# Performance work log

Measured on AMD Instinct MI355X. Metric: run time of the kernel, lower is better.

Reference implementation:

```python
import jax, jax.numpy as jnp
import numpy as np

B, L, S, E, D = 16, 2048, 2048, 64, 64

def setup_inputs() -> dict:
    key = jax.random.key(0)
    k1, k2, k3, k4 = jax.random.split(key, 4)
    queries = jax.random.normal(k1, (B, L, E), dtype=jnp.float32)
    keys = jax.random.normal(k2, (B, S, E), dtype=jnp.float32)
    values = jax.random.normal(k3, (B, S, D), dtype=jnp.float32)
    mlp = jax.random.normal(k4, (L, L), dtype=jnp.float32)  # learned seq-mix matrix
    return {"queries": queries, "keys": keys, "values": values, "mlp": mlp}

def reference(queries, keys, values, mlp):
    # scale = 1/sqrt(E) (self.scale is None)
    E_dim = queries.shape[-1]
    scale = 1.0 / jnp.sqrt(jnp.asarray(E_dim, dtype=queries.dtype))
    # scores: [B, L, S]
    scores = jnp.einsum('ble,bse->bls', queries, keys)
    # dropout omitted (eval mode / attention_dropout=0)
    A = jax.nn.softmax(scale * scores, axis=-1)
    # attention output: [B, L, D]
    V = jnp.einsum('bls,bsd->bld', A, values)
    # learned sequence-mixing: [B, L, D] -> [B, P, D] with P == L
    out = jnp.einsum('bld,pl->bpd', V, mlp)
    return out
```

## Files before the change

kernel.cpp:

```cpp
#include <hip/hip_runtime.h>

#define NB 16
#define NL 2048
#define NS 2048
#define NE 64
#define ND 64

typedef float floatx4 __attribute__((ext_vector_type(4)));
typedef _Float16 half8 __attribute__((ext_vector_type(8)));
typedef __fp16 half2v __attribute__((ext_vector_type(2)));

union H8 { half8 v; half2v h2[4]; };

__device__ __forceinline__ half8 cvt8(floatx4 a, floatx4 b) {
  H8 h;
  h.h2[0] = __builtin_amdgcn_cvt_pkrtz(a[0], a[1]);
  h.h2[1] = __builtin_amdgcn_cvt_pkrtz(a[2], a[3]);
  h.h2[2] = __builtin_amdgcn_cvt_pkrtz(b[0], b[1]);
  h.h2[3] = __builtin_amdgcn_cvt_pkrtz(b[2], b[3]);
  return h.v;
}

__device__ __forceinline__ void async16(void* l, const void* g) {
  __builtin_amdgcn_global_load_lds((__attribute__((address_space(1))) void*)g,
                                   (__attribute__((address_space(3))) void*)l, 16, 0, 0);
}

__device__ __forceinline__ int kinv(int y) {
  return (y & 0x23) | ((y & 8) << 1) | ((y & 4) << 1) | ((y & 16) >> 2);
}

__global__ __launch_bounds__(256) void prep_k(const float* __restrict__ V,
                                              const float* __restrict__ K,
                                              _Float16* __restrict__ Vt,
                                              _Float16* __restrict__ Kh,
                                              int do_k) {
  __shared__ __align__(16) _Float16 Vl[64][72];
  const int bid = blockIdx.x;
  const int t = threadIdx.x;

  if (bid < 512) {
    const int b = bid >> 5;
    const int s0 = (bid & 31) * 64;
    {
      int sl = t & 63;
      int dg = t >> 6;
      const float* src = V + ((size_t)(b * NS + s0 + sl)) * ND + dg * 16;
      int x = kinv(sl);
      #pragma unroll
      for (int c = 0; c < 4; ++c) {
        floatx4 v = *(const floatx4*)(src + c * 4);
        #pragma unroll
        for (int e = 0; e < 4; ++e) Vl[dg * 16 + c * 4 + e][x] = (_Float16)v[e];
      }
    }
    __syncthreads();
    {
      int d = t & 63;
      int xg = t >> 6;
      int dk = (d & 7) << 3;
      #pragma unroll
      for (int h = 0; h < 2; ++h) {
        int x = xg * 16 + h * 8;
        half8 v = *(const half8*)&Vl[d][x];
        *(half8*)(Vt + ((size_t)(b * ND + d)) * NS + s0 + (x ^ dk)) = v;
      }
    }
  } else {
    if (!do_k) return;
    int c = (bid - 512) * 256 + t;
    int j = c & 7;
    int s = (c >> 3) & (NS - 1);
    int b = c >> 14;
    const float* src = K + ((size_t)(b * NS + s)) * NE + j * 8;
    half8 h = cvt8(*(const floatx4*)src, *(const floatx4*)(src + 4));
    *(half8*)(Kh + ((size_t)(b * NS + s)) * NE + (j ^ (s & 7)) * 8) = h;
  }
}

template<bool KH16>
__global__ __launch_bounds__(512) void attn_k(const float* __restrict__ Q,
                                              const void* __restrict__ Ksrc,
                                              const _Float16* __restrict__ Vtp,
                                              _Float16* __restrict__ Vatt,
                                              const float* __restrict__ Mf,
                                              _Float16* __restrict__ Mh) {
  __shared__ __align__(16) char smem[98304];
  const int tid = threadIdx.x;
  const int wid = tid >> 6, lane = tid & 63;
  const int lr = lane & 15, lg = lane >> 4;
  const int g = wid & 1;
  const int qh = wid >> 1;
  const int L = blockIdx.y * 16 + blockIdx.x;
  const int b = (L & 7) * 2 + ((L >> 3) & 1);
  const int qx = L >> 4;
  const int qbase = qx * 128 + qh * 32;
  const _Float16* Kh = (const _Float16*)Ksrc;
  const float* Kf = (const float*)Ksrc;

  constexpr float SC = 0.18033688f;
  half8 qf[2][2];
  #pragma unroll
  for (int sub = 0; sub < 2; ++sub)
    #pragma unroll
    for (int kk = 0; kk < 2; ++kk) {
      const float* qp = Q + ((size_t)(b * NL + qbase + sub * 16 + lr)) * NE + kk * 32 + lg * 8;
      floatx4 a = *(const floatx4*)qp, c = *(const floatx4*)(qp + 4);
      qf[sub][kk] = cvt8(a * SC, c * SC);
    }

  half8 ones;
  #pragma unroll
  for (int i = 0; i < 8; ++i) ones[i] = (_Float16)1.0f;

  floatx4 oacc[2][4], lacc[2];
  #pragma unroll
  for (int s = 0; s < 2; ++s) {
    lacc[s] = (floatx4){0.f, 0.f, 0.f, 0.f};
    #pragma unroll
    for (int m = 0; m < 4; ++m) oacc[s][m] = (floatx4){0.f, 0.f, 0.f, 0.f};
  }

  int kOff[4][2], vOff[2][4];
  #pragma unroll
  for (int mt = 0; mt < 4; ++mt)
    #pragma unroll
    for (int kk = 0; kk < 2; ++kk) {
      int row = g * 64 + mt * 16 + lr, col = kk * 32 + lg * 8;
      kOff[mt][kk] = (row * 128 + col * 2) ^ ((row & 7) << 4);
    }
  #pragma unroll
  for (int kk = 0; kk < 2; ++kk)
    #pragma unroll
    for (int mt = 0; mt < 4; ++mt) {
      int row = mt * 16 + lr;
      vOff[kk][mt] = row * 256 + g * 128 + (((kk * 32 + lg * 8) * 2) ^ ((row & 7) << 4));
    }

  auto stageV = [&](int buf, int s0) {
    #pragma unroll
    for (int i = 0; i < 2; ++i) {
      int co = (wid * 2 + i) * 1024;
      int o = co + lane * 16;
      int row = o >> 8, c16 = (o >> 4) & 15;
      async16(smem + 49152 + buf * 16384 + co,
              Vtp + ((size_t)(b * ND + row)) * NS + s0 + c16 * 8);
    }
  };
  auto stageK = [&](int buf, int s0) {
    if constexpr (KH16) {
      #pragma unroll
      for (int i = 0; i < 2; ++i) {
        int co = (wid * 2 + i) * 1024;
        int o = co + lane * 16;
        int row = o >> 7, c8 = (o >> 4) & 7;
        async16(smem + buf * 16384 + co,
                Kh + ((size_t)(b * NS + s0 + row)) * NE + c8 * 8);
      }
    } else {
      int row = tid >> 2, cg = (tid & 3) * 16;
      const float* kp = Kf + ((size_t)(b * NS + s0 + row)) * NE + cg;
      #pragma unroll
      for (int c = 0; c < 2; ++c) {
        half8 h = cvt8(*(const floatx4*)(kp + c * 8), *(const floatx4*)(kp + c * 8 + 4));
        int col = cg + c * 8;
        *(half8*)(smem + buf * 16384 + ((row * 128 + col * 2) ^ ((row & 7) << 4))) = h;
      }
    }
  };

  stageK(0, 0); stageV(0, 0);

  int br = 0;
  for (int t = 0; t < NS / 128; ++t) {
    int bn = (br == 2) ? 0 : br + 1;
    if (t + 1 < NS / 128) {
      stageK(bn, (t + 1) * 128); stageV(bn, (t + 1) * 128);
      if constexpr (KH16) {
        asm volatile("s_waitcnt vmcnt(4)" ::: "memory");
        __builtin_amdgcn_s_barrier();
      } else __syncthreads();
    } else {
      if constexpr (KH16) {
        asm volatile("s_waitcnt vmcnt(0)" ::: "memory");
        __builtin_amdgcn_s_barrier();
      } else __syncthreads();
    }

    const char* kb = smem + br * 16384;
    const char* vb = smem + 49152 + br * 16384;

    half8 kf[4][2];
    #pragma unroll
    for (int mt = 0; mt < 4; ++mt)
      #pragma unroll
      for (int kk = 0; kk < 2; ++kk)
        kf[mt][kk] = *(const half8*)(kb + kOff[mt][kk]);

    H8 bf[2][2];
    #pragma unroll
    for (int sub = 0; sub < 2; ++sub) {
      floatx4 sacc[4];
      #pragma unroll
      for (int mt = 0; mt < 4; ++mt) sacc[mt] = (floatx4){0.f, 0.f, 0.f, 0.f};
      __builtin_amdgcn_s_setprio(1);
      #pragma unroll
      for (int kk = 0; kk < 2; ++kk)
        #pragma unroll
        for (int mt = 0; mt < 4; ++mt)
          sacc[mt] = __builtin_amdgcn_mfma_f32_16x16x32_f16(kf[mt][kk], qf[sub][kk], sacc[mt], 0, 0, 0);
      __builtin_amdgcn_s_setprio(0);

      #pragma unroll
      for (int mt = 0; mt < 4; ++mt) {
        float p0 = __builtin_amdgcn_exp2f(sacc[mt][0]);
        float p1 = __builtin_amdgcn_exp2f(sacc[mt][1]);
        float p2 = __builtin_amdgcn_exp2f(sacc[mt][2]);
        float p3 = __builtin_amdgcn_exp2f(sacc[mt][3]);
        bf[sub][mt >> 1].h2[(mt & 1) * 2]     = __builtin_amdgcn_cvt_pkrtz(p0, p1);
        bf[sub][mt >> 1].h2[(mt & 1) * 2 + 1] = __builtin_amdgcn_cvt_pkrtz(p2, p3);
      }
    }

    __builtin_amdgcn_s_setprio(1);
    #pragma unroll
    for (int kk = 0; kk < 2; ++kk) {
      #pragma unroll
      for (int mt = 0; mt < 4; ++mt) {
        half8 vt = *(const half8*)(vb + vOff[kk][mt]);
        oacc[0][mt] = __builtin_amdgcn_mfma_f32_16x16x32_f16(vt, bf[0][kk].v, oacc[0][mt], 0, 0, 0);
        oacc[1][mt] = __builtin_amdgcn_mfma_f32_16x16x32_f16(vt, bf[1][kk].v, oacc[1][mt], 0, 0, 0);
      }
      lacc[0] = __builtin_amdgcn_mfma_f32_16x16x32_f16(ones, bf[0][kk].v, lacc[0], 0, 0, 0);
      lacc[1] = __builtin_amdgcn_mfma_f32_16x16x32_f16(ones, bf[1][kk].v, lacc[1], 0, 0, 0);
    }
    __builtin_amdgcn_s_setprio(0);
    br = bn;
  }

  __syncthreads();

  {
    char* red = smem + qh * 12288;
    if (g == 1) {
      #pragma unroll
      for (int sub = 0; sub < 2; ++sub)
        #pragma unroll
        for (int mt = 0; mt < 4; ++mt)
          *(floatx4*)(red + lane * 144 + (sub * 4 + mt) * 16) = oacc[sub][mt];
      if (lg == 0) {
        *(float*)(red + 9216 + lr * 8) = lacc[0][0];
        *(float*)(red + 9216 + lr * 8 + 4) = lacc[1][0];
      }
    }
    __syncthreads();
    if (g == 0) {
      #pragma unroll
      for (int sub = 0; sub < 2; ++sub) {
        float lt = lacc[sub][0] + *(const float*)(red + 9216 + lr * 8 + sub * 4);
        float inv = __builtin_amdgcn_rcpf(lt);
        int l = qbase + sub * 16 + lr;
        #pragma unroll
        for (int mt = 0; mt < 4; ++mt) {
          floatx4 o = oacc[sub][mt] + *(const floatx4*)(red + lane * 144 + (sub * 4 + mt) * 16);
          #pragma unroll
          for (int r = 0; r < 4; ++r) {
            int d = mt * 16 + lg * 4 + r;
            int lsw = (l & ~63) | ((l & 63) ^ ((d & 7) << 3));
            Vatt[((size_t)(b * ND + d)) * NL + lsw] = (_Float16)(o[r] * inv);
          }
        }
      }
    }
  }

  if constexpr (KH16) {
    int mb = blockIdx.y * 16 + blockIdx.x;
    #pragma unroll
    for (int q = 0; q < 4; ++q) {
      int c = mb * 2048 + q * 512 + tid;
      int j = c & 255, p = c >> 8;
      const float* src = Mf + (size_t)p * NL + j * 8;
      half8 h = cvt8(*(const floatx4*)src, *(const floatx4*)(src + 4));
      int jo = (j & ~7) | ((j & 7) ^ (p & 7));
      *(half8*)(Mh + (size_t)p * NL + jo * 8) = h;
    }
  }
}

template<bool A16>
__global__ __launch_bounds__(256) void mix_k(const void* __restrict__ Asrc,
                                             const _Float16* __restrict__ Bsrc,
                                             float* __restrict__ out) {
  __shared__ __align__(16) char smem[65536];
  const int tid = threadIdx.x;
  const int wid = tid >> 6, lane = tid & 63;
  const int lr = lane & 15, lg = lane >> 4;
  const int kh = wid & 1;
  const int mw = wid >> 1;
  const int L = blockIdx.y * 32 + blockIdx.x;
  const int i = L >> 3;
  const int p0 = ((L & 7) * 4 + (i & 3)) * 64;
  const int b = i >> 2;
  const _Float16* Ah = (const _Float16*)Asrc;
  const float* Af = (const float*)Asrc;

  floatx4 acc[2][4];
  #pragma unroll
  for (int mt = 0; mt < 2; ++mt)
    #pragma unroll
    for (int nt = 0; nt < 4; ++nt) acc[mt][nt] = (floatx4){0.f, 0.f, 0.f, 0.f};

  auto stage = [&](int buf, int t) {
    int k0 = kh * (NL / 2) + t * 64;
    if constexpr (A16) {
      #pragma unroll
      for (int i2 = 0; i2 < 4; ++i2) {
        int co = (mw * 4 + i2) * 1024;
        int o = co + lane * 16;
        int row = o >> 7, c8 = (o >> 4) & 7;
        async16(smem + kh * 16384 + buf * 8192 + co,
                Ah + ((size_t)(p0 + row)) * NL + k0 + c8 * 8);
      }
    } else {
      int row = (lane & 31) + mw * 32, cg = (lane >> 5) * 32;
      const float* ap = Af + ((size_t)(p0 + row)) * NL + k0 + cg;
      #pragma unroll
      for (int c = 0; c < 4; ++c) {
        half8 h = cvt8(*(const floatx4*)(ap + c * 8), *(const floatx4*)(ap + c * 8 + 4));
        int col = cg + c * 8;
        *(half8*)(smem + kh * 16384 + buf * 8192 +
                  ((row * 128 + col * 2) ^ ((row & 7) << 4))) = h;
      }
    }
    #pragma unroll
    for (int i2 = 0; i2 < 4; ++i2) {
      int co = (mw * 4 + i2) * 1024;
      int o = co + lane * 16;
      int row = o >> 7, c8 = (o >> 4) & 7;
      async16(smem + 32768 + kh * 16384 + buf * 8192 + co,
              Bsrc + ((size_t)(b * ND + row)) * NL + k0 + c8 * 8);
    }
  };

  stage(0, 0);
  if constexpr (!A16) __syncthreads();

  for (int t = 0; t < 16; ++t) {
    int buf = t & 1;
    if constexpr (A16) {
      asm volatile("s_waitcnt vmcnt(0)" ::: "memory");
      __builtin_amdgcn_s_barrier();
      if (t + 1 < 16) stage(buf ^ 1, t + 1);
    } else {
      if (t + 1 < 16) { stage(buf ^ 1, t + 1); __syncthreads(); }
    }
    const char* ab = smem + kh * 16384 + buf * 8192;
    const char* bb = smem + 32768 + kh * 16384 + buf * 8192;
    #pragma unroll
    for (int kk = 0; kk < 2; ++kk) {
      int col = kk * 32 + lg * 8;
      half8 af[2];
      #pragma unroll
      for (int mt = 0; mt < 2; ++mt) {
        int row = mw * 32 + mt * 16 + lr;
        af[mt] = *(const half8*)(ab + ((row * 128 + col * 2) ^ ((row & 7) << 4)));
      }
      __builtin_amdgcn_s_setprio(1);
      #pragma unroll
      for (int nt = 0; nt < 4; ++nt) {
        int row = nt * 16 + lr;
        half8 bfr = *(const half8*)(bb + ((row * 128 + col * 2) ^ ((row & 7) << 4)));
        #pragma unroll
        for (int mt = 0; mt < 2; ++mt)
          acc[mt][nt] = __builtin_amdgcn_mfma_f32_16x16x32_f16(af[mt], bfr, acc[mt][nt], 0, 0, 0);
      }
      __builtin_amdgcn_s_setprio(0);
    }
    if constexpr (!A16) __syncthreads();
  }

  __syncthreads();

  if (kh == 1) {
    #pragma unroll
    for (int mt = 0; mt < 2; ++mt)
      #pragma unroll
      for (int nt = 0; nt < 4; ++nt) {
        int idx = mt * 4 + nt;
        *(floatx4*)(smem + mw * 8192 + lane * 128 + ((idx ^ (lane & 7)) * 16)) = acc[mt][nt];
      }
  }
  __syncthreads();
  if (kh == 0) {
    #pragma unroll
    for (int mt = 0; mt < 2; ++mt)
      #pragma unroll
      for (int nt = 0; nt < 4; ++nt) {
        int idx = mt * 4 + nt;
        acc[mt][nt] += *(const floatx4*)(smem + mw * 8192 + lane * 128 + ((idx ^ (lane & 7)) * 16));
        #pragma unroll
        for (int r = 0; r < 4; ++r) {
          int p = p0 + mw * 32 + mt * 16 + lg * 4 + r;
          int d = nt * 16 + lr;
          out[((size_t)(b * NL + p)) * ND + d] = acc[mt][nt][r];
        }
      }
  }
}

extern "C" void kernel_launch(void* const* d_in, const int* in_sizes, int n_in,
                              void* d_out, int out_size, void* d_ws, size_t ws_size,
                              hipStream_t stream) {
  (void)in_sizes; (void)n_in; (void)out_size;
  const float* Q = (const float*)d_in[0];
  const float* K = (const float*)d_in[1];
  const float* V = (const float*)d_in[2];
  const float* M = (const float*)d_in[3];
  float* out = (float*)d_out;

  char* ws = (char*)d_ws;
  _Float16* Vtp  = (_Float16*)ws;
  _Float16* Vatt = (_Float16*)(ws + (4u << 20));
  _Float16* Kh   = (_Float16*)(ws + (8u << 20));
  _Float16* Mh   = (_Float16*)(ws + (12u << 20));
  bool big = ws_size >= (size_t)(20u << 20);

  if (big) {
    prep_k<<<1536, 256, 0, stream>>>(V, K, Vtp, Kh, 1);
    attn_k<true><<<dim3(16, 16), 512, 0, stream>>>(Q, Kh, Vtp, Vatt, M, Mh);
    mix_k<true><<<dim3(32, 16), 256, 0, stream>>>(Mh, Vatt, out);
  } else {
    prep_k<<<512, 256, 0, stream>>>(V, K, Vtp, Kh, 0);
    attn_k<false><<<dim3(16, 16), 512, 0, stream>>>(Q, K, Vtp, Vatt, nullptr, nullptr);
    mix_k<false><<<dim3(32, 16), 256, 0, stream>>>(M, Vatt, out);
  }
}
```

Baseline: 51.83 us.

## Convert K to fp16 inside attention with register-prefetched loads, drop K prep pass

```diff
diff --git a/kernel.cpp b/kernel.cpp
--- a/kernel.cpp
+++ b/kernel.cpp
@@ -31,56 +31,41 @@
 }
 
 __global__ __launch_bounds__(256) void prep_k(const float* __restrict__ V,
-                                              const float* __restrict__ K,
-                                              _Float16* __restrict__ Vt,
-                                              _Float16* __restrict__ Kh,
-                                              int do_k) {
+                                              _Float16* __restrict__ Vt) {
   __shared__ __align__(16) _Float16 Vl[64][72];
   const int bid = blockIdx.x;
   const int t = threadIdx.x;
-
-  if (bid < 512) {
-    const int b = bid >> 5;
-    const int s0 = (bid & 31) * 64;
-    {
-      int sl = t & 63;
-      int dg = t >> 6;
-      const float* src = V + ((size_t)(b * NS + s0 + sl)) * ND + dg * 16;
-      int x = kinv(sl);
-      #pragma unroll
-      for (int c = 0; c < 4; ++c) {
-        floatx4 v = *(const floatx4*)(src + c * 4);
-        #pragma unroll
-        for (int e = 0; e < 4; ++e) Vl[dg * 16 + c * 4 + e][x] = (_Float16)v[e];
-      }
-    }
-    __syncthreads();
-    {
-      int d = t & 63;
-      int xg = t >> 6;
-      int dk = (d & 7) << 3;
-      #pragma unroll
-      for (int h = 0; h < 2; ++h) {
-        int x = xg * 16 + h * 8;
-        half8 v = *(const half8*)&Vl[d][x];
-        *(half8*)(Vt + ((size_t)(b * ND + d)) * NS + s0 + (x ^ dk)) = v;
-      }
-    }
-  } else {
-    if (!do_k) return;
-    int c = (bid - 512) * 256 + t;
-    int j = c & 7;
-    int s = (c >> 3) & (NS - 1);
-    int b = c >> 14;
-    const float* src = K + ((size_t)(b * NS + s)) * NE + j * 8;
-    half8 h = cvt8(*(const floatx4*)src, *(const floatx4*)(src + 4));
-    *(half8*)(Kh + ((size_t)(b * NS + s)) * NE + (j ^ (s & 7)) * 8) = h;
-  }
-}
-
-template<bool KH16>
+  const int b = bid >> 5;
+  const int s0 = (bid & 31) * 64;
+  {
+    int sl = t & 63;
+    int dg = t >> 6;
+    const float* src = V + ((size_t)(b * NS + s0 + sl)) * ND + dg * 16;
+    int x = kinv(sl);
+    #pragma unroll
+    for (int c = 0; c < 4; ++c) {
+      floatx4 v = *(const floatx4*)(src + c * 4);
+      #pragma unroll
+      for (int e = 0; e < 4; ++e) Vl[dg * 16 + c * 4 + e][x] = (_Float16)v[e];
+    }
+  }
+  __syncthreads();
+  {
+    int d = t & 63;
+    int xg = t >> 6;
+    int dk = (d & 7) << 3;
+    #pragma unroll
+    for (int h = 0; h < 2; ++h) {
+      int x = xg * 16 + h * 8;
+      half8 v = *(const half8*)&Vl[d][x];
+      *(half8*)(Vt + ((size_t)(b * ND + d)) * NS + s0 + (x ^ dk)) = v;
+    }
+  }
+}
+
+template<bool DOM>
 __global__ __launch_bounds__(512) void attn_k(const float* __restrict__ Q,
-                                              const void* __restrict__ Ksrc,
+                                              const float* __restrict__ Kf,
                                               const _Float16* __restrict__ Vtp,
                                               _Float16* __restrict__ Vatt,
                                               const float* __restrict__ Mf,
@@ -95,8 +80,6 @@
   const int b = (L & 7) * 2 + ((L >> 3) & 1);
   const int qx = L >> 4;
   const int qbase = qx * 128 + qh * 32;
-  const _Float16* Kh = (const _Float16*)Ksrc;
-  const float* Kf = (const float*)Ksrc;
 
   constexpr float SC = 0.18033688f;
   half8 qf[2][2];
@@ -136,6 +119,11 @@
       int row = mt * 16 + lr;
       vOff[kk][mt] = row * 256 + g * 128 + (((kk * 32 + lg * 8) * 2) ^ ((row & 7) << 4));
     }
+
+  const int krow = tid >> 2;
+  const int kcg = (tid & 3) * 16;
+  const int kw0 = (krow * 128 + kcg * 2) ^ ((krow & 7) << 4);
+  const int kw1 = (krow * 128 + (kcg + 8) * 2) ^ ((krow & 7) << 4);
 
   auto stageV = [&](int buf, int s0) {
     #pragma unroll
@@ -147,44 +135,31 @@
               Vtp + ((size_t)(b * ND + row)) * NS + s0 + c16 * 8);
     }
   };
-  auto stageK = [&](int buf, int s0) {
-    if constexpr (KH16) {
-      #pragma unroll
-      for (int i = 0; i < 2; ++i) {
-        int co = (wid * 2 + i) * 1024;
-        int o = co + lane * 16;
-        int row = o >> 7, c8 = (o >> 4) & 7;
-        async16(smem + buf * 16384 + co,
-                Kh + ((size_t)(b * NS + s0 + row)) * NE + c8 * 8);
-      }
-    } else {
-      int row = tid >> 2, cg = (tid & 3) * 16;
-      const float* kp = Kf + ((size_t)(b * NS + s0 + row)) * NE + cg;
-      #pragma unroll
-      for (int c = 0; c < 2; ++c) {
-        half8 h = cvt8(*(const floatx4*)(kp + c * 8), *(const floatx4*)(kp + c * 8 + 4));
-        int col = cg + c * 8;
-        *(half8*)(smem + buf * 16384 + ((row * 128 + col * 2) ^ ((row & 7) << 4))) = h;
-      }
-    }
-  };
-
-  stageK(0, 0); stageV(0, 0);
+
+  {
+    const float* kp = Kf + ((size_t)(b * NS + krow)) * NE + kcg;
+    floatx4 k0 = ((const floatx4*)kp)[0], k1 = ((const floatx4*)kp)[1];
+    floatx4 k2 = ((const floatx4*)kp)[2], k3 = ((const floatx4*)kp)[3];
+    *(half8*)(smem + kw0) = cvt8(k0, k1);
+    *(half8*)(smem + kw1) = cvt8(k2, k3);
+  }
+  stageV(0, 0);
 
   int br = 0;
   for (int t = 0; t < NS / 128; ++t) {
     int bn = (br == 2) ? 0 : br + 1;
+    floatx4 kr0, kr1, kr2, kr3;
     if (t + 1 < NS / 128) {
-      stageK(bn, (t + 1) * 128); stageV(bn, (t + 1) * 128);
-      if constexpr (KH16) {
-        asm volatile("s_waitcnt vmcnt(4)" ::: "memory");
-        __builtin_amdgcn_s_barrier();
-      } else __syncthreads();
+      const float* kp = Kf + ((size_t)(b * NS + (t + 1) * 128 + krow)) * NE + kcg;
+      kr0 = ((const floatx4*)kp)[0]; kr1 = ((const floatx4*)kp)[1];
+      kr2 = ((const floatx4*)kp)[2]; kr3 = ((const floatx4*)kp)[3];
+      stageV(bn, (t + 1) * 128);
+      asm volatile("s_waitcnt vmcnt(6) lgkmcnt(0)" ::: "memory");
+      __builtin_amdgcn_s_barrier();
     } else {
-      if constexpr (KH16) {
-        asm volatile("s_waitcnt vmcnt(0)" ::: "memory");
-        __builtin_amdgcn_s_barrier();
-      } else __syncthreads();
+      kr0 = kr1 = kr2 = kr3 = (floatx4){0.f, 0.f, 0.f, 0.f};
+      asm volatile("s_waitcnt vmcnt(0) lgkmcnt(0)" ::: "memory");
+      __builtin_amdgcn_s_barrier();
     }
 
     const char* kb = smem + br * 16384;
@@ -235,6 +210,12 @@
       lacc[1] = __builtin_amdgcn_mfma_f32_16x16x32_f16(ones, bf[1][kk].v, lacc[1], 0, 0, 0);
     }
     __builtin_amdgcn_s_setprio(0);
+
+    if (t + 1 < NS / 128) {
+      asm volatile("s_waitcnt vmcnt(2)" ::: "memory");
+      *(half8*)(smem + bn * 16384 + kw0) = cvt8(kr0, kr1);
+      *(half8*)(smem + bn * 16384 + kw1) = cvt8(kr2, kr3);
+    }
     br = bn;
   }
 
@@ -274,7 +255,7 @@
     }
   }
 
-  if constexpr (KH16) {
+  if constexpr (DOM) {
     int mb = blockIdx.y * 16 + blockIdx.x;
     #pragma unroll
     for (int q = 0; q < 4; ++q) {
@@ -422,16 +403,14 @@
   char* ws = (char*)d_ws;
   _Float16* Vtp  = (_Float16*)ws;
   _Float16* Vatt = (_Float16*)(ws + (4u << 20));
-  _Float16* Kh   = (_Float16*)(ws + (8u << 20));
-  _Float16* Mh   = (_Float16*)(ws + (12u << 20));
-  bool big = ws_size >= (size_t)(20u << 20);
-
+  _Float16* Mh   = (_Float16*)(ws + (8u << 20));
+  bool big = ws_size >= (size_t)(16u << 20);
+
+  prep_k<<<512, 256, 0, stream>>>(V, Vtp);
   if (big) {
-    prep_k<<<1536, 256, 0, stream>>>(V, K, Vtp, Kh, 1);
-    attn_k<true><<<dim3(16, 16), 512, 0, stream>>>(Q, Kh, Vtp, Vatt, M, Mh);
+    attn_k<true><<<dim3(16, 16), 512, 0, stream>>>(Q, K, Vtp, Vatt, M, Mh);
     mix_k<true><<<dim3(32, 16), 256, 0, stream>>>(Mh, Vatt, out);
   } else {
-    prep_k<<<512, 256, 0, stream>>>(V, K, Vtp, Kh, 0);
     attn_k<false><<<dim3(16, 16), 512, 0, stream>>>(Q, K, Vtp, Vatt, nullptr, nullptr);
     mix_k<false><<<dim3(32, 16), 256, 0, stream>>>(M, Vatt, out);
   }
```

Result: slower. 52.98 us (+2.2%).
